# Optimization experiments

Measured on AMD Instinct MI355X. Metric: run time of the kernel, lower is better.

Reference implementation:

```python
import jax, jax.numpy as jnp
import numpy as np

N_NODES = 20000
N_EDGES = 640000
DIM_NODE = 256
DIM_EDGE = 128
N_CENTERS = 64
DIM_HIDDEN = 128


def setup_inputs() -> dict:
    key = jax.random.key(0)
    ks = jax.random.split(key, 12)
    inp = {
        "node_h": jax.random.normal(ks[0], (N_NODES, DIM_NODE), dtype=jnp.float32),
        "edge_h": jax.random.normal(ks[1], (N_EDGES, DIM_EDGE), dtype=jnp.float32),
        "dist": jax.random.normal(ks[2], (N_EDGES, N_CENTERS), dtype=jnp.float32),
        "src": jax.random.randint(ks[3], (N_EDGES,), 0, N_NODES, dtype=jnp.int32),
        "dst": jax.random.randint(ks[4], (N_EDGES,), 0, N_NODES, dtype=jnp.int32),
        # learned params (nn.Linear: y = x @ W.T + b; we store W already transposed)
        "W_node": jax.random.normal(ks[5], (DIM_NODE, DIM_HIDDEN), dtype=jnp.float32) / np.sqrt(DIM_NODE),
        "b_node": jnp.zeros((DIM_HIDDEN,), dtype=jnp.float32),
        "W_edge": jax.random.normal(ks[6], (DIM_EDGE, DIM_HIDDEN), dtype=jnp.float32) / np.sqrt(DIM_EDGE),
        "b_edge": jnp.zeros((DIM_HIDDEN,), dtype=jnp.float32),
        "W_dist": jax.random.normal(ks[7], (N_CENTERS, DIM_HIDDEN), dtype=jnp.float32) / np.sqrt(N_CENTERS),
        "b_dist": jnp.zeros((DIM_HIDDEN,), dtype=jnp.float32),
        "W_comb": jax.random.normal(ks[8], (2 * DIM_HIDDEN, DIM_NODE), dtype=jnp.float32) / np.sqrt(2 * DIM_HIDDEN),
    }
    return inp


def reference(node_h, edge_h, dist, src, dst,
              W_node, b_node, W_edge, b_edge, W_dist, b_dist, W_comb):
    # fc_node is per-node: compute once on [N, dim_node], then gather per edge
    node_proj = node_h @ W_node + b_node            # [N, H]
    m1 = node_proj[src] * (dist @ W_dist + b_dist)  # [E, H]
    m2 = edge_h @ W_edge + b_edge                   # [E, H]
    m = jnp.tanh(jnp.concatenate([m1, m2], axis=1) @ W_comb)  # [E, dim_node]
    # scatter-sum into destination nodes (DGL reduce: mailbox sum)
    h = jax.ops.segment_sum(m, dst, num_segments=N_NODES)     # [N, dim_node]
    # per-node L2 normalization (norm=True)
    h = h / jnp.linalg.norm(h, axis=1, keepdims=True)
    return h
```

## Files before the change

kernel.cpp:

```cpp
#include <hip/hip_runtime.h>
#include <hip/hip_bf16.h>
#include <math.h>

typedef __attribute__((ext_vector_type(4))) float fx4;
typedef __attribute__((ext_vector_type(8))) short bx8;
typedef __attribute__((ext_vector_type(4))) short bx4;

#define DEV static __device__ __forceinline__
#define N_NODES 20000
#define N_EDGES 640000

DEV unsigned short f2bf(float f){
  __hip_bfloat16 h = __float2bfloat16(f);
  return *(unsigned short*)&h;
}
DEV float bf2f(unsigned short h){
  union { float f; unsigned u; } a; a.u = ((unsigned)h) << 16;
  return a.f;
}
DEV float fast_tanh(float x){
  return 1.0f - 2.0f / (__expf(2.0f * x) + 1.0f);
}
DEV bx8 cvt8(fx4 a, fx4 b){
  bx8 r;
  r[0]=(short)f2bf(a[0]); r[1]=(short)f2bf(a[1]); r[2]=(short)f2bf(a[2]); r[3]=(short)f2bf(a[3]);
  r[4]=(short)f2bf(b[0]); r[5]=(short)f2bf(b[1]); r[6]=(short)f2bf(b[2]); r[7]=(short)f2bf(b[3]);
  return r;
}

__global__ __launch_bounds__(256)
void prep_kernel(const float* __restrict__ Wn, const float* __restrict__ Wd,
                 unsigned short* __restrict__ WnP, unsigned short* __restrict__ WdP)
{
  int t = blockIdx.x * 256 + threadIdx.x;
  if (t >= 40960) return;
  const float* W; unsigned short* P; int i, ks, nblk;
  if (t < 32768) { W=Wn; P=WnP; i=t;        ks=(i>>9)&7; nblk=i>>12; }
  else           { W=Wd; P=WdP; i=t-32768;  ks=(i>>9)&1; nblk=i>>10; }
  int j    = i & 7;
  int lane = (i >> 3) & 63;
  int k = ks*32 + (lane>>4)*8 + j;
  int n = nblk*16 + (lane&15);
  P[i] = f2bf(W[k*128 + n]);
}

__global__ __launch_bounds__(256)
void prep2_kernel(const float* __restrict__ We, const float* __restrict__ Wc,
                  const float* __restrict__ be,
                  unsigned short* __restrict__ WctP, unsigned short* __restrict__ WeffP,
                  float* __restrict__ ceff)
{
  int t = blockIdx.x * 256 + threadIdx.x;
  if (t < 32768){
    int i=t, j=i&7, lane=(i>>3)&63, ks=(i>>9)&3, nblk=i>>11;
    int k = ks*32 + (lane>>4)*8 + j;
    int n = nblk*16 + (lane&15);
    WctP[i] = f2bf(Wc[k*256 + n]);
  } else if (t < 65536){
    int i=t-32768, j=i&7, lane=(i>>3)&63, ks=(i>>9)&3, nblk=i>>11;
    int k = ks*32 + (lane>>4)*8 + j;
    int n = nblk*16 + (lane&15);
    float s = 0.f;
    for (int h = 0; h < 128; ++h)
      s += We[k*128 + h] * Wc[(128+h)*256 + n];
    WeffP[i] = f2bf(s);
  } else if (t < 65792){
    int n = t - 65536;
    float s = 0.f;
    for (int h = 0; h < 128; ++h)
      s += be[h] * Wc[(128+h)*256 + n];
    ceff[n] = s;
  }
}

__global__ __launch_bounds__(256)
void hist_kernel(const int* __restrict__ dst, int* __restrict__ cnt)
{
  int e = blockIdx.x * 256 + threadIdx.x;
  if (e < N_EDGES) atomicAdd(&cnt[dst[e]], 1);
}

__global__ __launch_bounds__(1024)
void scan_kernel(const int* __restrict__ cnt, int* __restrict__ fill)
{
  __shared__ int wsum[16];
  __shared__ int carry_s;
  const int t = threadIdx.x, lane = t & 63, w = t >> 6;
  if (t == 0) carry_s = 0;
  __syncthreads();
  for (int c = 0; c < 20; ++c){
    int i = c*1024 + t;
    int v = (i < N_NODES) ? cnt[i] : 0;
    int x = v;
#pragma unroll
    for (int s = 1; s < 64; s <<= 1){
      int u = __shfl_up(x, s, 64);
      if (lane >= s) x += u;
    }
    if (lane == 63) wsum[w] = x;
    __syncthreads();
    if (w == 0 && lane < 16){
      int y = wsum[lane];
#pragma unroll
      for (int s = 1; s < 16; s <<= 1){
        int u = __shfl_up(y, s, 64);
        if (lane >= s) y += u;
      }
      wsum[lane] = y;
    }
    __syncthreads();
    int wbase = (w == 0) ? 0 : wsum[w-1];
    int excl = carry_s + wbase + x - v;
    if (i < N_NODES) fill[i] = excl;
    __syncthreads();
    if (t == 1023) carry_s = excl + v;
    __syncthreads();
  }
}

__global__ __launch_bounds__(256)
void scatter_kernel(const int* __restrict__ dst, int* __restrict__ fill,
                    int* __restrict__ perm, int* __restrict__ dstS)
{
  int e = blockIdx.x * 256 + threadIdx.x;
  if (e < N_EDGES){
    int d = dst[e];
    int pos = atomicAdd(&fill[d], 1);
    perm[pos] = e;
    dstS[pos] = d;
  }
}

__global__ __launch_bounds__(64)
void node_proj_kernel(const float* __restrict__ node_h, const unsigned short* __restrict__ WnP,
                      const float* __restrict__ b_node, unsigned short* __restrict__ npj)
{
  __shared__ unsigned short sN[16 * 264];
  const int lane = threadIdx.x;
  const int lr = lane & 15, lq = lane >> 4;
  const long r0 = (long)blockIdx.x * 16;

  const fx4* g = (const fx4*)(node_h + r0 * 256);
#pragma unroll
  for (int i = 0; i < 16; ++i){
    int idx = lane + 64 * i;
    int r = idx >> 6, c4 = idx & 63;
    fx4 v = g[idx];
    bx4 b;
    b[0]=(short)f2bf(v[0]); b[1]=(short)f2bf(v[1]); b[2]=(short)f2bf(v[2]); b[3]=(short)f2bf(v[3]);
    *(bx4*)&sN[r*264 + c4*4] = b;
  }
  __syncthreads();

  fx4 acc[8];
#pragma unroll
  for (int n = 0; n < 8; ++n) acc[n] = (fx4){0.f,0.f,0.f,0.f};
#pragma unroll
  for (int ks = 0; ks < 8; ++ks){
    bx8 a = *(const bx8*)&sN[lr*264 + ks*32 + lq*8];
#pragma unroll
    for (int n = 0; n < 8; ++n){
      bx8 b = *(const bx8*)&WnP[((n*8 + ks)*64 + lane)*8];
      acc[n] = __builtin_amdgcn_mfma_f32_16x16x32_bf16(a, b, acc[n], 0, 0, 0);
    }
  }
#pragma unroll
  for (int n = 0; n < 8; ++n){
    float bias = b_node[n*16 + lr];
#pragma unroll
    for (int j = 0; j < 4; ++j)
      npj[(r0 + lq*4 + j)*128 + n*16 + lr] = f2bf(acc[n][j] + bias);
  }
}

__global__ __launch_bounds__(256, 3)
void edge_kernel(const float* __restrict__ edge_h, const float* __restrict__ dist,
                 const int* __restrict__ src,
                 const int* __restrict__ perm, const int* __restrict__ dstS,
                 const unsigned short* __restrict__ npj,
                 const unsigned short* __restrict__ WdP, const float* __restrict__ b_dist,
                 const unsigned short* __restrict__ WctP, const unsigned short* __restrict__ WeffP,
                 const float* __restrict__ ceff,
                 float* __restrict__ hacc)
{
  __shared__ unsigned short sX[4][16*136];
  __shared__ unsigned short sE[4][16*136];

  const int tid  = threadIdx.x;
  const int w    = tid >> 6;
  const int lane = tid & 63;
  const int lr   = lane & 15;
  const int lq   = lane >> 4;
  const int c32  = lane & 31;
  const long e0  = (long)blockIdx.x * 64;

  int vPerm = 0, vSrc = 0;
  if (lane < 16){
    int p = perm[e0 + w*16 + lane];
    vPerm = p;
    vSrc  = src[p];
  }
  const int vDst = dstS[e0 + lane];
  const int pRow = __shfl(vPerm, lr);

  bx4 rN[8];
#pragma unroll
  for (int i = 0; i < 8; ++i){
    int r = (lane >> 5) + 2*i;
    int s = __shfl(vSrc, r);
    rN[i] = *(const bx4*)(npj + (long)s*128 + c32*4);
  }

  fx4 rE[8];
#pragma unroll
  for (int i = 0; i < 8; ++i){
    int r = (lane >> 5) + 2*i;
    int p = __shfl(vPerm, r);
    rE[i] = *(const fx4*)(edge_h + (long)p*128 + c32*4);
  }

  {
    const float* dp = dist + (long)pRow*64 + lq*8;
    fx4 d0 = *(const fx4*)(dp);
    fx4 d1 = *(const fx4*)(dp + 4);
    fx4 d2 = *(const fx4*)(dp + 32);
    fx4 d3 = *(const fx4*)(dp + 36);
    bx8 a0 = cvt8(d0, d1);
    bx8 a1 = cvt8(d2, d3);
    fx4 facc[8];
#pragma unroll
    for (int n = 0; n < 8; ++n) facc[n] = (fx4){0.f,0.f,0.f,0.f};
#pragma unroll
    for (int n = 0; n < 8; ++n){
      bx8 b = *(const bx8*)&WdP[((n*2 + 0)*64 + lane)*8];
      facc[n] = __builtin_amdgcn_mfma_f32_16x16x32_bf16(a0, b, facc[n], 0, 0, 0);
    }
#pragma unroll
    for (int n = 0; n < 8; ++n){
      bx8 b = *(const bx8*)&WdP[((n*2 + 1)*64 + lane)*8];
      facc[n] = __builtin_amdgcn_mfma_f32_16x16x32_bf16(a1, b, facc[n], 0, 0, 0);
    }
#pragma unroll
    for (int n = 0; n < 8; ++n)
#pragma unroll
      for (int j = 0; j < 4; ++j)
        sX[w][(lq*4 + j)*136 + n*16 + lr] = f2bf(facc[n][j]);
  }

  {
    const fx4 bd = *(const fx4*)(b_dist + c32*4);
#pragma unroll
    for (int i = 0; i < 8; ++i){
      int r = (lane >> 5) + 2*i;
      bx4 dp4 = *(const bx4*)&sX[w][r*136 + c32*4];
      bx4 o;
#pragma unroll
      for (int k = 0; k < 4; ++k)
        o[k] = (short)f2bf( bf2f((unsigned short)rN[i][k]) * (bf2f((unsigned short)dp4[k]) + bd[k]) );
      *(bx4*)&sX[w][r*136 + c32*4] = o;
    }
  }

#pragma unroll
  for (int i = 0; i < 8; ++i){
    int r = (lane >> 5) + 2*i;
    bx4 cv;
    cv[0]=(short)f2bf(rE[i][0]); cv[1]=(short)f2bf(rE[i][1]);
    cv[2]=(short)f2bf(rE[i][2]); cv[3]=(short)f2bf(rE[i][3]);
    *(bx4*)&sE[w][r*136 + c32*4] = cv;
  }
  __syncthreads();

  fx4 acc[4][4];
#pragma unroll
  for (int rt = 0; rt < 4; ++rt)
#pragma unroll
    for (int n = 0; n < 4; ++n) acc[rt][n] = (fx4){0.f,0.f,0.f,0.f};
#pragma unroll
  for (int ks = 0; ks < 4; ++ks){
    bx8 a[4], b[4];
#pragma unroll
    for (int rt = 0; rt < 4; ++rt)
      a[rt] = *(const bx8*)&sX[rt][lr*136 + ks*32 + lq*8];
#pragma unroll
    for (int n = 0; n < 4; ++n)
      b[n] = *(const bx8*)&WctP[(((4*w + n)*4 + ks)*64 + lane)*8];
#pragma unroll
    for (int rt = 0; rt < 4; ++rt)
#pragma unroll
      for (int n = 0; n < 4; ++n)
        acc[rt][n] = __builtin_amdgcn_mfma_f32_16x16x32_bf16(a[rt], b[n], acc[rt][n], 0, 0, 0);
  }
#pragma unroll
  for (int ks = 0; ks < 4; ++ks){
    bx8 a[4], b[4];
#pragma unroll
    for (int rt = 0; rt < 4; ++rt)
      a[rt] = *(const bx8*)&sE[rt][lr*136 + ks*32 + lq*8];
#pragma unroll
    for (int n = 0; n < 4; ++n)
      b[n] = *(const bx8*)&WeffP[(((4*w + n)*4 + ks)*64 + lane)*8];
#pragma unroll
    for (int rt = 0; rt < 4; ++rt)
#pragma unroll
      for (int n = 0; n < 4; ++n)
        acc[rt][n] = __builtin_amdgcn_mfma_f32_16x16x32_bf16(a[rt], b[n], acc[rt][n], 0, 0, 0);
  }

  float ce[4];
#pragma unroll
  for (int n = 0; n < 4; ++n) ce[n] = ceff[(4*w + n)*16 + lr];
#pragma unroll
  for (int rt = 0; rt < 4; ++rt)
#pragma unroll
    for (int n = 0; n < 4; ++n)
#pragma unroll
      for (int j = 0; j < 4; ++j)
        acc[rt][n][j] = fast_tanh(acc[rt][n][j] + ce[n]);

  {
    int up = __shfl_up(vDst, 1);
    bool head = (lane == 0) || (up != vDst);
    unsigned long long m = __ballot(head);
    while (m){
      int lo = __ffsll((unsigned long long)m) - 1;
      m &= m - 1;
      int hi = m ? (__ffsll((unsigned long long)m) - 1) : 64;
      int d  = __shfl(vDst, lo);
      float s0=0.f, s1=0.f, s2=0.f, s3=0.f;
#pragma unroll
      for (int rt = 0; rt < 4; ++rt)
#pragma unroll
        for (int j = 0; j < 4; ++j){
          int row = rt*16 + lq*4 + j;
          float msk = (row >= lo && row < hi) ? 1.f : 0.f;
          s0 += msk * acc[rt][0][j];
          s1 += msk * acc[rt][1][j];
          s2 += msk * acc[rt][2][j];
          s3 += msk * acc[rt][3][j];
        }
      s0 += __shfl_xor(s0, 16); s0 += __shfl_xor(s0, 32);
      s1 += __shfl_xor(s1, 16); s1 += __shfl_xor(s1, 32);
      s2 += __shfl_xor(s2, 16); s2 += __shfl_xor(s2, 32);
      s3 += __shfl_xor(s3, 16); s3 += __shfl_xor(s3, 32);
      float v = (lq == 0) ? s0 : (lq == 1) ? s1 : (lq == 2) ? s2 : s3;
      float* p = &hacc[(long)d*256 + (4*w + lq)*16 + lr];
      if (lo == 0 || hi == 64) atomicAdd(p, v);
      else                     *p = v;
    }
  }
}

__global__ __launch_bounds__(256)
void norm_kernel(float* __restrict__ h)
{
  int row  = blockIdx.x * 4 + (threadIdx.x >> 6);
  int lane = threadIdx.x & 63;
  fx4 v = *(const fx4*)&h[(long)row*256 + lane*4];
  float s = v[0]*v[0] + v[1]*v[1] + v[2]*v[2] + v[3]*v[3];
#pragma unroll
  for (int off = 32; off > 0; off >>= 1) s += __shfl_xor(s, off);
  float inv = (s > 0.f) ? 1.0f / sqrtf(s) : 0.f;
  v[0]*=inv; v[1]*=inv; v[2]*=inv; v[3]*=inv;
  *(fx4*)&h[(long)row*256 + lane*4] = v;
}

extern "C" void kernel_launch(void* const* d_in, const int* in_sizes, int n_in,
                              void* d_out, int out_size, void* d_ws, size_t ws_size,
                              hipStream_t stream)
{
  const float* node_h = (const float*)d_in[0];
  const float* edge_h = (const float*)d_in[1];
  const float* dist   = (const float*)d_in[2];
  const int*   src    = (const int*)d_in[3];
  const int*   dst    = (const int*)d_in[4];
  const float* W_node = (const float*)d_in[5];
  const float* b_node = (const float*)d_in[6];
  const float* W_edge = (const float*)d_in[7];
  const float* b_edge = (const float*)d_in[8];
  const float* W_dist = (const float*)d_in[9];
  const float* b_dist = (const float*)d_in[10];
  const float* W_comb = (const float*)d_in[11];

  char* ws = (char*)d_ws;
  unsigned short* npj   = (unsigned short*)ws;
  unsigned short* WnP   = (unsigned short*)(ws + 5120000);
  unsigned short* WdP   = (unsigned short*)(ws + 5185536);
  unsigned short* WctP  = (unsigned short*)(ws + 5201920);
  unsigned short* WeffP = (unsigned short*)(ws + 5267456);
  float*          ceff  = (float*)(ws + 5332992);
  int* cnt  = (int*)(ws + 5334016);
  int* fill = (int*)(ws + 5414016);
  int* perm = (int*)(ws + 5494016);
  int* dstS = (int*)(ws + 8054016);

  float* hacc = (float*)d_out;

  hipMemsetAsync(hacc, 0, (size_t)N_NODES * 256 * sizeof(float), stream);
  hipMemsetAsync(cnt, 0, (size_t)N_NODES * sizeof(int), stream);

  prep_kernel<<<160, 256, 0, stream>>>(W_node, W_dist, WnP, WdP);
  prep2_kernel<<<257, 256, 0, stream>>>(W_edge, W_comb, b_edge, WctP, WeffP, ceff);
  hist_kernel<<<2500, 256, 0, stream>>>(dst, cnt);
  scan_kernel<<<1, 1024, 0, stream>>>(cnt, fill);
  scatter_kernel<<<2500, 256, 0, stream>>>(dst, fill, perm, dstS);
  node_proj_kernel<<<1250, 64, 0, stream>>>(node_h, WnP, b_node, npj);
  edge_kernel<<<10000, 256, 0, stream>>>(edge_h, dist, src, perm, dstS, npj,
                                         WdP, b_dist, WctP, WeffP, ceff, hacc);
  norm_kernel<<<5000, 256, 0, stream>>>(hacc);
}
```

Baseline: 389.7 us.

## Split edge kernel output columns into two halves to raise occupancy

Splits the combine GEMM, tanh and segmented scatter into two passes over half of each wave's output columns, shrinking the live accumulator set so the kernel can target 4 blocks per CU instead of 3. It also folds b_dist into the MFMA accumulator init, reorders the global loads so edge_h and dist are issued early, and replaces the tanh division with a hardware reciprocal. The trade-off is that the segment reduction loop now runs twice with half the lanes idle on stores, A fragments are reloaded from LDS twice, and the tighter register budget may cause spills.

```diff
diff --git a/kernel.cpp b/kernel.cpp
--- a/kernel.cpp
+++ b/kernel.cpp
@@ -19,7 +19,8 @@
   return a.f;
 }
 DEV float fast_tanh(float x){
-  return 1.0f - 2.0f / (__expf(2.0f * x) + 1.0f);
+  float t = __expf(2.0f * x);
+  return 1.0f - 2.0f * __builtin_amdgcn_rcpf(t + 1.0f);
 }
 DEV bx8 cvt8(fx4 a, fx4 b){
   bx8 r;
@@ -173,7 +174,7 @@
   }
 }
 
-__global__ __launch_bounds__(256, 3)
+__global__ __launch_bounds__(256, 4)
 void edge_kernel(const float* __restrict__ edge_h, const float* __restrict__ dist,
                  const int* __restrict__ src,
                  const int* __restrict__ perm, const int* __restrict__ dstS,
@@ -203,6 +204,14 @@
   const int vDst = dstS[e0 + lane];
   const int pRow = __shfl(vPerm, lr);
 
+  fx4 rE[8];
+#pragma unroll
+  for (int i = 0; i < 8; ++i){
+    int r = (lane >> 5) + 2*i;
+    int p = __shfl(vPerm, r);
+    rE[i] = *(const fx4*)(edge_h + (long)p*128 + c32*4);
+  }
+
   bx4 rN[8];
 #pragma unroll
   for (int i = 0; i < 8; ++i){
@@ -211,55 +220,11 @@
     rN[i] = *(const bx4*)(npj + (long)s*128 + c32*4);
   }
 
-  fx4 rE[8];
-#pragma unroll
-  for (int i = 0; i < 8; ++i){
-    int r = (lane >> 5) + 2*i;
-    int p = __shfl(vPerm, r);
-    rE[i] = *(const fx4*)(edge_h + (long)p*128 + c32*4);
-  }
-
-  {
-    const float* dp = dist + (long)pRow*64 + lq*8;
-    fx4 d0 = *(const fx4*)(dp);
-    fx4 d1 = *(const fx4*)(dp + 4);
-    fx4 d2 = *(const fx4*)(dp + 32);
-    fx4 d3 = *(const fx4*)(dp + 36);
-    bx8 a0 = cvt8(d0, d1);
-    bx8 a1 = cvt8(d2, d3);
-    fx4 facc[8];
-#pragma unroll
-    for (int n = 0; n < 8; ++n) facc[n] = (fx4){0.f,0.f,0.f,0.f};
-#pragma unroll
-    for (int n = 0; n < 8; ++n){
-      bx8 b = *(const bx8*)&WdP[((n*2 + 0)*64 + lane)*8];
-      facc[n] = __builtin_amdgcn_mfma_f32_16x16x32_bf16(a0, b, facc[n], 0, 0, 0);
-    }
-#pragma unroll
-    for (int n = 0; n < 8; ++n){
-      bx8 b = *(const bx8*)&WdP[((n*2 + 1)*64 + lane)*8];
-      facc[n] = __builtin_amdgcn_mfma_f32_16x16x32_bf16(a1, b, facc[n], 0, 0, 0);
-    }
-#pragma unroll
-    for (int n = 0; n < 8; ++n)
-#pragma unroll
-      for (int j = 0; j < 4; ++j)
-        sX[w][(lq*4 + j)*136 + n*16 + lr] = f2bf(facc[n][j]);
-  }
-
-  {
-    const fx4 bd = *(const fx4*)(b_dist + c32*4);
-#pragma unroll
-    for (int i = 0; i < 8; ++i){
-      int r = (lane >> 5) + 2*i;
-      bx4 dp4 = *(const bx4*)&sX[w][r*136 + c32*4];
-      bx4 o;
-#pragma unroll
-      for (int k = 0; k < 4; ++k)
-        o[k] = (short)f2bf( bf2f((unsigned short)rN[i][k]) * (bf2f((unsigned short)dp4[k]) + bd[k]) );
-      *(bx4*)&sX[w][r*136 + c32*4] = o;
-    }
-  }
+  const float* dp = dist + (long)pRow*64 + lq*8;
+  fx4 d0 = *(const fx4*)(dp);
+  fx4 d1 = *(const fx4*)(dp + 4);
+  fx4 d2 = *(const fx4*)(dp + 32);
+  fx4 d3 = *(const fx4*)(dp + 36);
 
 #pragma unroll
   for (int i = 0; i < 8; ++i){
@@ -269,65 +234,104 @@
     cv[2]=(short)f2bf(rE[i][2]); cv[3]=(short)f2bf(rE[i][3]);
     *(bx4*)&sE[w][r*136 + c32*4] = cv;
   }
+
+  {
+    bx8 a0 = cvt8(d0, d1);
+    bx8 a1 = cvt8(d2, d3);
+    fx4 facc[8];
+#pragma unroll
+    for (int n = 0; n < 8; ++n){
+      float bdv = b_dist[n*16 + lr];
+      facc[n] = (fx4){bdv, bdv, bdv, bdv};
+    }
+#pragma unroll
+    for (int n = 0; n < 8; ++n){
+      bx8 b = *(const bx8*)&WdP[((n*2 + 0)*64 + lane)*8];
+      facc[n] = __builtin_amdgcn_mfma_f32_16x16x32_bf16(a0, b, facc[n], 0, 0, 0);
+    }
+#pragma unroll
+    for (int n = 0; n < 8; ++n){
+      bx8 b = *(const bx8*)&WdP[((n*2 + 1)*64 + lane)*8];
+      facc[n] = __builtin_amdgcn_mfma_f32_16x16x32_bf16(a1, b, facc[n], 0, 0, 0);
+    }
+#pragma unroll
+    for (int n = 0; n < 8; ++n)
+#pragma unroll
+      for (int j = 0; j < 4; ++j)
+        sX[w][(lq*4 + j)*136 + n*16 + lr] = f2bf(facc[n][j]);
+  }
+
+#pragma unroll
+  for (int i = 0; i < 8; ++i){
+    int r = (lane >> 5) + 2*i;
+    bx4 dp4 = *(const bx4*)&sX[w][r*136 + c32*4];
+    bx4 o;
+#pragma unroll
+    for (int k = 0; k < 4; ++k)
+      o[k] = (short)f2bf( bf2f((unsigned short)rN[i][k]) * bf2f((unsigned short)dp4[k]) );
+    *(bx4*)&sX[w][r*136 + c32*4] = o;
+  }
   __syncthreads();
 
-  fx4 acc[4][4];
-#pragma unroll
-  for (int rt = 0; rt < 4; ++rt)
-#pragma unroll
-    for (int n = 0; n < 4; ++n) acc[rt][n] = (fx4){0.f,0.f,0.f,0.f};
-#pragma unroll
-  for (int ks = 0; ks < 4; ++ks){
-    bx8 a[4], b[4];
+  int up = __shfl_up(vDst, 1);
+  bool head = (lane == 0) || (up != vDst);
+  const unsigned long long mhead = __ballot(head);
+
+#pragma unroll
+  for (int h = 0; h < 2; ++h){
+    fx4 acc[4][2];
 #pragma unroll
     for (int rt = 0; rt < 4; ++rt)
-      a[rt] = *(const bx8*)&sX[rt][lr*136 + ks*32 + lq*8];
-#pragma unroll
-    for (int n = 0; n < 4; ++n)
-      b[n] = *(const bx8*)&WctP[(((4*w + n)*4 + ks)*64 + lane)*8];
+#pragma unroll
+      for (int n = 0; n < 2; ++n) acc[rt][n] = (fx4){0.f,0.f,0.f,0.f};
+#pragma unroll
+    for (int ks = 0; ks < 4; ++ks){
+      bx8 a[4], b[2];
+#pragma unroll
+      for (int rt = 0; rt < 4; ++rt)
+        a[rt] = *(const bx8*)&sX[rt][lr*136 + ks*32 + lq*8];
+#pragma unroll
+      for (int n = 0; n < 2; ++n)
+        b[n] = *(const bx8*)&WctP[(((4*w + 2*h + n)*4 + ks)*64 + lane)*8];
+#pragma unroll
+      for (int rt = 0; rt < 4; ++rt)
+#pragma unroll
+        for (int n = 0; n < 2; ++n)
+          acc[rt][n] = __builtin_amdgcn_mfma_f32_16x16x32_bf16(a[rt], b[n], acc[rt][n], 0, 0, 0);
+    }
+#pragma unroll
+    for (int ks = 0; ks < 4; ++ks){
+      bx8 a[4], b[2];
+#pragma unroll
+      for (int rt = 0; rt < 4; ++rt)
+        a[rt] = *(const bx8*)&sE[rt][lr*136 + ks*32 + lq*8];
+#pragma unroll
+      for (int n = 0; n < 2; ++n)
+        b[n] = *(const bx8*)&WeffP[(((4*w + 2*h + n)*4 + ks)*64 + lane)*8];
+#pragma unroll
+      for (int rt = 0; rt < 4; ++rt)
+#pragma unroll
+        for (int n = 0; n < 2; ++n)
+          acc[rt][n] = __builtin_amdgcn_mfma_f32_16x16x32_bf16(a[rt], b[n], acc[rt][n], 0, 0, 0);
+    }
+
+    float ce0 = ceff[(4*w + 2*h + 0)*16 + lr];
+    float ce1 = ceff[(4*w + 2*h + 1)*16 + lr];
 #pragma unroll
     for (int rt = 0; rt < 4; ++rt)
 #pragma unroll
-      for (int n = 0; n < 4; ++n)
-        acc[rt][n] = __builtin_amdgcn_mfma_f32_16x16x32_bf16(a[rt], b[n], acc[rt][n], 0, 0, 0);
-  }
-#pragma unroll
-  for (int ks = 0; ks < 4; ++ks){
-    bx8 a[4], b[4];
-#pragma unroll
-    for (int rt = 0; rt < 4; ++rt)
-      a[rt] = *(const bx8*)&sE[rt][lr*136 + ks*32 + lq*8];
-#pragma unroll
-    for (int n = 0; n < 4; ++n)
-      b[n] = *(const bx8*)&WeffP[(((4*w + n)*4 + ks)*64 + lane)*8];
-#pragma unroll
-    for (int rt = 0; rt < 4; ++rt)
-#pragma unroll
-      for (int n = 0; n < 4; ++n)
-        acc[rt][n] = __builtin_amdgcn_mfma_f32_16x16x32_bf16(a[rt], b[n], acc[rt][n], 0, 0, 0);
-  }
-
-  float ce[4];
-#pragma unroll
-  for (int n = 0; n < 4; ++n) ce[n] = ceff[(4*w + n)*16 + lr];
-#pragma unroll
-  for (int rt = 0; rt < 4; ++rt)
-#pragma unroll
-    for (int n = 0; n < 4; ++n)
-#pragma unroll
-      for (int j = 0; j < 4; ++j)
-        acc[rt][n][j] = fast_tanh(acc[rt][n][j] + ce[n]);
-
-  {
-    int up = __shfl_up(vDst, 1);
-    bool head = (lane == 0) || (up != vDst);
-    unsigned long long m = __ballot(head);
+      for (int j = 0; j < 4; ++j){
+        acc[rt][0][j] = fast_tanh(acc[rt][0][j] + ce0);
+        acc[rt][1][j] = fast_tanh(acc[rt][1][j] + ce1);
+      }
+
+    unsigned long long m = mhead;
     while (m){
       int lo = __ffsll((unsigned long long)m) - 1;
       m &= m - 1;
       int hi = m ? (__ffsll((unsigned long long)m) - 1) : 64;
       int d  = __shfl(vDst, lo);
-      float s0=0.f, s1=0.f, s2=0.f, s3=0.f;
+      float s0 = 0.f, s1 = 0.f;
 #pragma unroll
       for (int rt = 0; rt < 4; ++rt)
 #pragma unroll
@@ -336,17 +340,15 @@
           float msk = (row >= lo && row < hi) ? 1.f : 0.f;
           s0 += msk * acc[rt][0][j];
           s1 += msk * acc[rt][1][j];
-          s2 += msk * acc[rt][2][j];
-          s3 += msk * acc[rt][3][j];
         }
       s0 += __shfl_xor(s0, 16); s0 += __shfl_xor(s0, 32);
       s1 += __shfl_xor(s1, 16); s1 += __shfl_xor(s1, 32);
-      s2 += __shfl_xor(s2, 16); s2 += __shfl_xor(s2, 32);
-      s3 += __shfl_xor(s3, 16); s3 += __shfl_xor(s3, 32);
-      float v = (lq == 0) ? s0 : (lq == 1) ? s1 : (lq == 2) ? s2 : s3;
-      float* p = &hacc[(long)d*256 + (4*w + lq)*16 + lr];
-      if (lo == 0 || hi == 64) atomicAdd(p, v);
-      else                     *p = v;
+      if (lq < 2){
+        float v = (lq == 0) ? s0 : s1;
+        float* p = &hacc[(long)d*256 + (4*w + 2*h + lq)*16 + lr];
+        if (lo == 0 || hi == 64) atomicAdd(p, v);
+        else                     *p = v;
+      }
     }
   }
 }
```

Result: faster. 379.6 us (-2.6%).
